# Kernel optimization log

Hardware: AMD Instinct MI355X
Metric: run time of the kernel (lower is better)

## Reference

```python
import jax, jax.numpy as jnp
import numpy as np

B, S, D, H = 2, 2048, 1024, 16
HD = D // H          # head dim = 64
BASE = 10000.0
SCALE = 1.0 / np.sqrt(HD)


def setup_inputs() -> dict:
    key = jax.random.key(0)
    ks = jax.random.split(key, 7)
    mk = lambda k, shp: (jax.random.normal(k, shp, dtype=jnp.float32) * 0.02)
    return {
        "hidden_states": jax.random.normal(ks[0], (B, S, D), dtype=jnp.float32),
        "Wq": mk(ks[1], (D, D)), "bq": jnp.zeros((D,), jnp.float32),
        "Wk": mk(ks[2], (D, D)), "bk": jnp.zeros((D,), jnp.float32),
        "Wv": mk(ks[3], (D, D)), "bv": jnp.zeros((D,), jnp.float32),
    }


def _rope_tables(seq_len, head_dim, dtype):
    # Intended RoPE: inv_freq over head_dim/2 frequencies.
    # (Original torch code has an off-by-2 indexing bug that makes it un-runnable
    #  for head_dim > 2; we implement the intended standard RoPE:
    #  inv_freq = base^{-arange(0, head_dim, 2)/head_dim}, length head_dim//2.)
    dim_half = head_dim // 2
    inv_freq = 1.0 / (BASE ** (jnp.arange(dim_half, dtype=dtype) / dim_half))
    ang = jnp.arange(seq_len, dtype=dtype)[:, None] * inv_freq[None, :]  # [S, dim_half]
    return jnp.sin(ang), jnp.cos(ang)


def _apply_rope(x, sin, cos):
    # x: [B, H, S, HD]; sin/cos: [S, HD//2]
    dim_half = x.shape[-1] // 2
    x1, x2 = x[..., :dim_half], x[..., dim_half:]
    sin = sin[None, None]  # [1,1,S,dim_half]
    cos = cos[None, None]
    return jnp.concatenate([x1 * cos - x2 * sin, x1 * sin + x2 * cos], axis=-1)


def reference(hidden_states, Wq, bq, Wk, bk, Wv, bv):
    b, s, d = hidden_states.shape
    # QKV projections (nn.Linear: x @ W.T + b), then split heads -> [B,H,S,HD]
    def proj(W, bias):
        y = jnp.einsum("bsd,ed->bse", hidden_states, W) + bias
        return y.reshape(b, s, H, HD).transpose(0, 2, 1, 3)

    q, k, v = proj(Wq, bq), proj(Wk, bk), proj(Wv, bv)

    sin, cos = _rope_tables(s, HD, hidden_states.dtype)
    q = _apply_rope(q, sin, cos)
    k = _apply_rope(k, sin, cos)

    # Non-causal SDPA, scale = 1/sqrt(head_dim), no mask, eval mode (no dropout)
    scores = jnp.einsum("bhqd,bhkd->bhqk", q, k) * SCALE
    probs = jax.nn.softmax(scores, axis=-1)
    ctx = jnp.einsum("bhqk,bhkd->bhqd", probs, v)

    # [B,H,S,HD] -> [B,S,D]
    return ctx.transpose(0, 2, 1, 3).reshape(b, s, d)
```

## Files before the change

kernel.cpp:

```cpp
#include <hip/hip_runtime.h>
#include <hip/hip_bf16.h>
#include <math.h>

#define B_  2
#define S_  2048
#define D_  1024
#define H_  16
#define HD_ 64
#define M_  (B_*S_)
#define N3  (3*D_)
#define K_  D_
#define LOG2E 1.44269504088896340736f

typedef unsigned short u16;
typedef __bf16 bf16x8 __attribute__((ext_vector_type(8)));
typedef float  f32x4  __attribute__((ext_vector_type(4)));
typedef float  f32x16 __attribute__((ext_vector_type(16)));
typedef unsigned short u16x4 __attribute__((ext_vector_type(4)));
typedef unsigned short u16x8 __attribute__((ext_vector_type(8)));
typedef unsigned int   u32x4v __attribute__((ext_vector_type(4)));

typedef const __attribute__((address_space(1))) unsigned int gu32;
typedef __attribute__((address_space(3)))       unsigned int lu32;

__device__ __forceinline__ void gload_lds16(const void* g, void* l) {
  __builtin_amdgcn_global_load_lds((gu32*)g, (lu32*)l, 16, 0, 0);
}

__device__ __forceinline__ u16 f2bf(float f) {
  unsigned u = __builtin_bit_cast(unsigned, f);
  u += 0x7fffu + ((u >> 16) & 1u);
  return (u16)(u >> 16);
}

__device__ __forceinline__ unsigned pk2(float lo, float hi) {
  unsigned d;
  asm("v_cvt_pk_bf16_f32 %0, %1, %2" : "=v"(d) : "v"(lo), "v"(hi));
  return d;
}

__global__ void k_prep(const float* __restrict__ hs, const float* __restrict__ Wq,
                       const float* __restrict__ Wk, const float* __restrict__ Wv,
                       u16* __restrict__ Xb, u16* __restrict__ Wb) {
  const int NX = M_*D_/4, NW = D_*D_/4;
  int i = blockIdx.x * blockDim.x + threadIdx.x;
  const float4* src; u16* dst; int off;
  if (i < NX)            { src = (const float4*)hs; dst = Xb;           off = i; }
  else if (i < NX+NW)    { src = (const float4*)Wq; dst = Wb;           off = i-NX; }
  else if (i < NX+2*NW)  { src = (const float4*)Wk; dst = Wb + D_*D_;   off = i-NX-NW; }
  else                   { src = (const float4*)Wv; dst = Wb + 2*D_*D_; off = i-NX-2*NW; }
  float4 v = src[off];
  ushort4 o; o.x = f2bf(v.x); o.y = f2bf(v.y); o.z = f2bf(v.z); o.w = f2bf(v.w);
  reinterpret_cast<ushort4*>(dst)[off] = o;
}

__global__ void k_tables(float* __restrict__ sinT, float* __restrict__ cosT) {
  int gid = blockIdx.x * blockDim.x + threadIdx.x;
  int s = gid >> 5, j = gid & 31;
  float invf = (float)exp(-(double)j * (log(10000.0) / 32.0));
  float angf = (float)s * invf;
  double ang = (double)angf;
  sinT[gid] = (float)sin(ang);
  cosT[gid] = (float)cos(ang);
}

#define BM 128
#define BN 128
#define BK 64

__global__ __launch_bounds__(256) void k_gemm(const u16* __restrict__ A,
                                              const u16* __restrict__ Bm,
                                              const float* __restrict__ bq,
                                              const float* __restrict__ bk,
                                              const float* __restrict__ bv,
                                              const float* __restrict__ sinT,
                                              const float* __restrict__ cosT,
                                              u16* __restrict__ Qo,
                                              u16* __restrict__ Ko,
                                              u16* __restrict__ Vo) {
  __shared__ alignas(16) u16 As[BM*BK];
  __shared__ alignas(16) u16 Bs[BN*BK];
  const int t = threadIdx.x;
  const int l = t & 63, w = t >> 6;
  const int wr = w >> 1, wc = w & 1;
  const int lr = l & 15, lg = l >> 4;
  const int m0 = blockIdx.y * BM, n0 = blockIdx.x * BN;

  f32x4 acc[4][4] = {};

  for (int k0 = 0; k0 < K_; k0 += BK) {
#pragma unroll
    for (int i = 0; i < 4; ++i) {
      int chunk = i*256 + t;
      int row = chunk >> 3, kc = chunk & 7;
      gload_lds16(A + (size_t)(m0+row)*K_ + k0 + kc*8, &As[chunk*8]);
    }
#pragma unroll
    for (int i = 0; i < 4; ++i) {
      int chunk = i*256 + t;
      int row = chunk >> 3, kc = chunk & 7;
      gload_lds16(Bm + (size_t)(n0+row)*K_ + k0 + kc*8, &Bs[chunk*8]);
    }
    __syncthreads();
#pragma unroll
    for (int ks = 0; ks < 2; ++ks) {
      bf16x8 a[4], b[4];
#pragma unroll
      for (int m = 0; m < 4; ++m)
        a[m] = *reinterpret_cast<const bf16x8*>(&As[(wr*64 + m*16 + lr)*BK + ks*32 + lg*8]);
#pragma unroll
      for (int n = 0; n < 4; ++n)
        b[n] = *reinterpret_cast<const bf16x8*>(&Bs[(wc*64 + n*16 + lr)*BK + ks*32 + lg*8]);
#pragma unroll
      for (int m = 0; m < 4; ++m)
#pragma unroll
        for (int n = 0; n < 4; ++n)
          acc[m][n] = __builtin_amdgcn_mfma_f32_16x16x32_bf16(a[m], b[n], acc[m][n], 0, 0, 0);
    }
    __syncthreads();
  }

  const int cw0  = n0 + wc*64;
  const int proj = cw0 >> 10;
  const int h    = (cw0 & (D_-1)) >> 6;
  const int b    = m0 >> 11;
  const int sb_  = (m0 & (S_-1)) + wr*64;

  if (proj < 2) {
    const float* bias = proj ? bk : bq;
    u16* dst = proj ? Ko : Qo;
    const float qs = proj ? 1.0f : 0.125f * LOG2E;
    float b1[2], b2[2];
#pragma unroll
    for (int n = 0; n < 2; ++n) {
      b1[n] = bias[h*HD_ + n*16 + lr];
      b2[n] = bias[h*HD_ + n*16 + lr + 32];
    }
#pragma unroll
    for (int m = 0; m < 4; ++m)
#pragma unroll
      for (int r = 0; r < 4; ++r) {
        int s = sb_ + m*16 + lg*4 + r;
        size_t orow = ((size_t)(b*H_ + h)*S_ + s)*HD_;
#pragma unroll
        for (int n = 0; n < 2; ++n) {
          int j = n*16 + lr;
          float x1 = acc[m][n][r]   + b1[n];
          float x2 = acc[m][n+2][r] + b2[n];
          float c  = cosT[(s<<5) + j], sn = sinT[(s<<5) + j];
          dst[orow + j]      = f2bf((x1*c - x2*sn) * qs);
          dst[orow + j + 32] = f2bf((x1*sn + x2*c) * qs);
        }
      }
  } else {
    float bb[4];
#pragma unroll
    for (int n = 0; n < 4; ++n) bb[n] = bv[h*HD_ + n*16 + lr];
#pragma unroll
    for (int m = 0; m < 4; ++m)
#pragma unroll
      for (int r = 0; r < 4; ++r) {
        int s = sb_ + m*16 + lg*4 + r;
        size_t orow = ((size_t)(b*H_ + h)*S_ + s)*HD_;
#pragma unroll
        for (int n = 0; n < 4; ++n)
          Vo[orow + n*16 + lr] = f2bf(acc[m][n][r] + bb[n]);
      }
  }
}

__global__ __launch_bounds__(256) void k_vt2(const u16* __restrict__ Vb,
                                             u16* __restrict__ Vt) {
  __shared__ u16 tile[64*68];
  const int bh = blockIdx.y, s0 = blockIdx.x * 64, t = threadIdx.x;
#pragma unroll
  for (int i = 0; i < 2; ++i) {
    int chunk = i*256 + t;
    int sl = chunk >> 3, c8 = chunk & 7;
    u16x8 v = *reinterpret_cast<const u16x8*>(Vb + ((size_t)bh*S_ + s0 + sl)*HD_ + c8*8);
    u16x4 lo = __builtin_shufflevector(v, v, 0, 1, 2, 3);
    u16x4 hi = __builtin_shufflevector(v, v, 4, 5, 6, 7);
    *reinterpret_cast<u16x4*>(&tile[sl*68 + c8*8])     = lo;
    *reinterpret_cast<u16x4*>(&tile[sl*68 + c8*8 + 4]) = hi;
  }
  __syncthreads();
#pragma unroll
  for (int i = 0; i < 2; ++i) {
    int chunk = i*256 + t;
    int hd = chunk >> 3, sb = chunk & 7;
    u16x8 o;
#pragma unroll
    for (int k = 0; k < 8; ++k) {
      int p   = sb*8 + k;
      int key = (p & ~15) | (p & 3) | ((p & 4) << 1) | ((p & 8) >> 1);
      o[k] = tile[key*68 + hd];
    }
    *reinterpret_cast<u16x8*>(Vt + ((size_t)bh*HD_ + hd)*S_ + s0 + sb*8) = o;
  }
}

#define QBW 32
#define NWV 4
#define QTT (QBW*NWV)
#define KTL 64
#define NTL (S_/KTL)

__global__ __launch_bounds__(256) void k_attn(const u16* __restrict__ Q,
                                              const u16* __restrict__ K,
                                              const u16* __restrict__ Vt,
                                              float* __restrict__ out) {
  __shared__ alignas(16) u16 Ks[2][KTL*HD_];
  __shared__ alignas(16) u16 Vs[2][HD_*KTL];
  __shared__ float lsums[NWV][QBW];
  const int t = threadIdx.x, l = t & 63, w = t >> 6;
  const int q32 = l & 31, hi = l >> 5;

  const int bid = blockIdx.x;
  const int work = (bid & 7) * 64 + (bid >> 3);
  const int bh = work >> 4;
  const int q0 = (work & 15) * QTT;

  const u16* Qg = Q  + ((size_t)bh*S_ + q0 + w*QBW)*HD_;
  const u16* Kg = K  + (size_t)bh*S_*HD_;
  const u16* Vg = Vt + (size_t)bh*HD_*S_;

  bf16x8 qf[4];
#pragma unroll
  for (int kt = 0; kt < 4; ++kt)
    qf[kt] = *reinterpret_cast<const bf16x8*>(Qg + (size_t)q32*HD_ + kt*16 + hi*8);

  f32x16 O0 = {}, O1 = {};
  float lsum = 0.f;

  const int srow = t >> 3, sg = t & 7;
  const int sg1 = sg ^ (srow & 7);
  const u16* kq = Kg + (size_t)srow*HD_ + sg1*8;
  const u16* vq = Vg + (size_t)srow*S_  + sg1*8;

  gload_lds16(kq,            &Ks[0][t*8]);
  gload_lds16(kq + 32*HD_,   &Ks[0][2048 + t*8]);
  gload_lds16(vq,            &Vs[0][t*8]);
  gload_lds16(vq + 32*S_,    &Vs[0][2048 + t*8]);
  __syncthreads();

  int cur = 0;
  for (int tile = 0; tile < NTL; ++tile) {
    if (tile + 1 < NTL) {
      const u16* kn = kq + (size_t)(tile+1)*KTL*HD_;
      const u16* vn = vq + (tile+1)*KTL;
      gload_lds16(kn,          &Ks[cur^1][t*8]);
      gload_lds16(kn + 32*HD_, &Ks[cur^1][2048 + t*8]);
      gload_lds16(vn,          &Vs[cur^1][t*8]);
      gload_lds16(vn + 32*S_,  &Vs[cur^1][2048 + t*8]);
    }

    f32x16 d0 = {}, d1 = {};
    __builtin_amdgcn_s_setprio(1);
#pragma unroll
    for (int kt = 0; kt < 4; ++kt) {
      const int gsw = ((kt*2 + hi) ^ (q32 & 7)) * 8;
      bf16x8 k0 = *reinterpret_cast<const bf16x8*>(&Ks[cur][q32*HD_ + gsw]);
      d0 = __builtin_amdgcn_mfma_f32_32x32x16_bf16(k0, qf[kt], d0, 0, 0, 0);
      bf16x8 k1 = *reinterpret_cast<const bf16x8*>(&Ks[cur][(32 + q32)*HD_ + gsw]);
      d1 = __builtin_amdgcn_mfma_f32_32x32x16_bf16(k1, qf[kt], d1, 0, 0, 0);
    }
    __builtin_amdgcn_s_setprio(0);

    unsigned pw[4][4];
#pragma unroll
    for (int c = 0; c < 4; ++c) {
      float e[8];
#pragma unroll
      for (int i = 0; i < 8; ++i) {
        float sv = (c < 2) ? d0[(c & 1)*8 + i] : d1[(c & 1)*8 + i];
        e[i] = exp2f(sv);
        lsum += e[i];
      }
#pragma unroll
      for (int j = 0; j < 4; ++j) pw[c][j] = pk2(e[2*j], e[2*j+1]);
    }

    __builtin_amdgcn_s_setprio(1);
#pragma unroll
    for (int c = 0; c < 4; ++c) {
      u32x4v pv_ = {pw[c][0], pw[c][1], pw[c][2], pw[c][3]};
      bf16x8 pa = __builtin_bit_cast(bf16x8, pv_);
      const int gv = ((c*2 + hi) ^ (q32 & 7)) * 8;
      bf16x8 v0 = *reinterpret_cast<const bf16x8*>(&Vs[cur][q32*KTL + gv]);
      O0 = __builtin_amdgcn_mfma_f32_32x32x16_bf16(pa, v0, O0, 0, 0, 0);
      bf16x8 v1 = *reinterpret_cast<const bf16x8*>(&Vs[cur][(32 + q32)*KTL + gv]);
      O1 = __builtin_amdgcn_mfma_f32_32x32x16_bf16(pa, v1, O1, 0, 0, 0);
    }
    __builtin_amdgcn_s_setprio(0);

    __syncthreads();
    cur ^= 1;
  }

  lsum += __shfl_xor(lsum, 32);
  if (l < 32) lsums[w][l] = lsum;

  const int b = bh >> 4, h = bh & 15;
#pragma unroll
  for (int r = 0; r < 16; ++r) {
    int qrow = (r & 3) + 8*(r >> 2) + 4*hi;
    float inv = 1.f / lsums[w][qrow];
    size_t o = (size_t)(b*S_ + q0 + w*QBW + qrow)*D_ + h*HD_;
    out[o + q32]      = O0[r] * inv;
    out[o + 32 + q32] = O1[r] * inv;
  }
}

extern "C" void kernel_launch(void* const* d_in, const int* in_sizes, int n_in,
                              void* d_out, int out_size, void* d_ws, size_t ws_size,
                              hipStream_t stream) {
  const float* hs = (const float*)d_in[0];
  const float* Wq = (const float*)d_in[1];
  const float* bq = (const float*)d_in[2];
  const float* Wk = (const float*)d_in[3];
  const float* bk = (const float*)d_in[4];
  const float* Wv = (const float*)d_in[5];
  const float* bv = (const float*)d_in[6];
  float* out = (float*)d_out;

  char* ws = (char*)d_ws;
  u16*   Xb   = (u16*)  (ws);
  u16*   Wb   = (u16*)  (ws + 8388608);
  u16*   Qb   = (u16*)  (ws + 14680064);
  u16*   Kb   = (u16*)  (ws + 23068672);
  u16*   Vb   = (u16*)  (ws + 31457280);
  u16*   Vtb  = (u16*)  (ws + 39845888);
  float* sinT = (float*)(ws + 48234496);
  float* cosT = (float*)(ws + 48496640);

  k_prep<<<(M_*D_/4 + 3*(D_*D_/4)) / 256, 256, 0, stream>>>(hs, Wq, Wk, Wv, Xb, Wb);
  k_tables<<<256, 256, 0, stream>>>(sinT, cosT);
  k_gemm<<<dim3(N3/BN, M_/BM), 256, 0, stream>>>(Xb, Wb, bq, bk, bv, sinT, cosT, Qb, Kb, Vb);
  k_vt2<<<dim3(S_/64, B_*H_), 256, 0, stream>>>(Vb, Vtb);
  k_attn<<<512, 256, 0, stream>>>(Qb, Kb, Vtb, out);
}
```

Before: 206.7 us.

## Double attention key tile to 128 and swizzle GEMM block order

```diff
diff --git a/kernel.cpp b/kernel.cpp
--- a/kernel.cpp
+++ b/kernel.cpp
@@ -84,7 +84,10 @@
   const int l = t & 63, w = t >> 6;
   const int wr = w >> 1, wc = w & 1;
   const int lr = l & 15, lg = l >> 4;
-  const int m0 = blockIdx.y * BM, n0 = blockIdx.x * BN;
+
+  const int lin = blockIdx.y * (N3/BN) + blockIdx.x;
+  const int wk  = (lin & 7) * 96 + (lin >> 3);
+  const int m0 = (wk / (N3/BN)) * BM, n0 = (wk % (N3/BN)) * BN;
 
   f32x4 acc[4][4] = {};
 
@@ -202,7 +205,7 @@
 #define QBW 32
 #define NWV 4
 #define QTT (QBW*NWV)
-#define KTL 64
+#define KTL 128
 #define NTL (S_/KTL)
 
 __global__ __launch_bounds__(256) void k_attn(const u16* __restrict__ Q,
@@ -232,66 +235,74 @@
   f32x16 O0 = {}, O1 = {};
   float lsum = 0.f;
 
-  const int srow = t >> 3, sg = t & 7;
-  const int sg1 = sg ^ (srow & 7);
-  const u16* kq = Kg + (size_t)srow*HD_ + sg1*8;
-  const u16* vq = Vg + (size_t)srow*S_  + sg1*8;
-
-  gload_lds16(kq,            &Ks[0][t*8]);
-  gload_lds16(kq + 32*HD_,   &Ks[0][2048 + t*8]);
-  gload_lds16(vq,            &Vs[0][t*8]);
-  gload_lds16(vq + 32*S_,    &Vs[0][2048 + t*8]);
+  const u16* ksrc[4]; const u16* vsrc[4];
+#pragma unroll
+  for (int i = 0; i < 4; ++i) {
+    int g  = t + 256*i;
+    int kr = g >> 3,  kc = (g & 7)  ^ (kr & 7);
+    ksrc[i] = Kg + (size_t)kr*HD_ + kc*8;
+    int vr = g >> 4,  vc = (g & 15) ^ (vr & 15);
+    vsrc[i] = Vg + (size_t)vr*S_ + vc*8;
+  }
+
+#pragma unroll
+  for (int i = 0; i < 4; ++i) {
+    gload_lds16(ksrc[i], &Ks[0][(t + 256*i)*8]);
+    gload_lds16(vsrc[i], &Vs[0][(t + 256*i)*8]);
+  }
   __syncthreads();
 
   int cur = 0;
   for (int tile = 0; tile < NTL; ++tile) {
     if (tile + 1 < NTL) {
-      const u16* kn = kq + (size_t)(tile+1)*KTL*HD_;
-      const u16* vn = vq + (tile+1)*KTL;
-      gload_lds16(kn,          &Ks[cur^1][t*8]);
-      gload_lds16(kn + 32*HD_, &Ks[cur^1][2048 + t*8]);
-      gload_lds16(vn,          &Vs[cur^1][t*8]);
-      gload_lds16(vn + 32*S_,  &Vs[cur^1][2048 + t*8]);
-    }
-
-    f32x16 d0 = {}, d1 = {};
-    __builtin_amdgcn_s_setprio(1);
-#pragma unroll
-    for (int kt = 0; kt < 4; ++kt) {
-      const int gsw = ((kt*2 + hi) ^ (q32 & 7)) * 8;
-      bf16x8 k0 = *reinterpret_cast<const bf16x8*>(&Ks[cur][q32*HD_ + gsw]);
-      d0 = __builtin_amdgcn_mfma_f32_32x32x16_bf16(k0, qf[kt], d0, 0, 0, 0);
-      bf16x8 k1 = *reinterpret_cast<const bf16x8*>(&Ks[cur][(32 + q32)*HD_ + gsw]);
-      d1 = __builtin_amdgcn_mfma_f32_32x32x16_bf16(k1, qf[kt], d1, 0, 0, 0);
-    }
-    __builtin_amdgcn_s_setprio(0);
-
-    unsigned pw[4][4];
-#pragma unroll
-    for (int c = 0; c < 4; ++c) {
-      float e[8];
-#pragma unroll
-      for (int i = 0; i < 8; ++i) {
-        float sv = (c < 2) ? d0[(c & 1)*8 + i] : d1[(c & 1)*8 + i];
-        e[i] = exp2f(sv);
-        lsum += e[i];
-      }
-#pragma unroll
-      for (int j = 0; j < 4; ++j) pw[c][j] = pk2(e[2*j], e[2*j+1]);
-    }
-
-    __builtin_amdgcn_s_setprio(1);
-#pragma unroll
-    for (int c = 0; c < 4; ++c) {
-      u32x4v pv_ = {pw[c][0], pw[c][1], pw[c][2], pw[c][3]};
-      bf16x8 pa = __builtin_bit_cast(bf16x8, pv_);
-      const int gv = ((c*2 + hi) ^ (q32 & 7)) * 8;
-      bf16x8 v0 = *reinterpret_cast<const bf16x8*>(&Vs[cur][q32*KTL + gv]);
-      O0 = __builtin_amdgcn_mfma_f32_32x32x16_bf16(pa, v0, O0, 0, 0, 0);
-      bf16x8 v1 = *reinterpret_cast<const bf16x8*>(&Vs[cur][(32 + q32)*KTL + gv]);
-      O1 = __builtin_amdgcn_mfma_f32_32x32x16_bf16(pa, v1, O1, 0, 0, 0);
-    }
-    __builtin_amdgcn_s_setprio(0);
+#pragma unroll
+      for (int i = 0; i < 4; ++i) {
+        gload_lds16(ksrc[i] + (size_t)(tile+1)*KTL*HD_, &Ks[cur^1][(t + 256*i)*8]);
+        gload_lds16(vsrc[i] + (tile+1)*KTL,             &Vs[cur^1][(t + 256*i)*8]);
+      }
+    }
+
+#pragma unroll
+    for (int half = 0; half < 2; ++half) {
+      f32x16 d0 = {}, d1 = {};
+      __builtin_amdgcn_s_setprio(1);
+#pragma unroll
+      for (int kt = 0; kt < 4; ++kt) {
+        const int gsw = ((kt*2 + hi) ^ (q32 & 7)) * 8;
+        bf16x8 k0 = *reinterpret_cast<const bf16x8*>(&Ks[cur][(half*64 + q32)*HD_ + gsw]);
+        d0 = __builtin_amdgcn_mfma_f32_32x32x16_bf16(k0, qf[kt], d0, 0, 0, 0);
+        bf16x8 k1 = *reinterpret_cast<const bf16x8*>(&Ks[cur][(half*64 + 32 + q32)*HD_ + gsw]);
+        d1 = __builtin_amdgcn_mfma_f32_32x32x16_bf16(k1, qf[kt], d1, 0, 0, 0);
+      }
+      __builtin_amdgcn_s_setprio(0);
+
+      unsigned pw[4][4];
+#pragma unroll
+      for (int c = 0; c < 4; ++c) {
+        float e[8];
+#pragma unroll
+        for (int i = 0; i < 8; ++i) {
+          float sv = (c < 2) ? d0[(c & 1)*8 + i] : d1[(c & 1)*8 + i];
+          e[i] = exp2f(sv);
+          lsum += e[i];
+        }
+#pragma unroll
+        for (int j = 0; j < 4; ++j) pw[c][j] = pk2(e[2*j], e[2*j+1]);
+      }
+
+      __builtin_amdgcn_s_setprio(1);
+#pragma unroll
+      for (int c = 0; c < 4; ++c) {
+        u32x4v pv_ = {pw[c][0], pw[c][1], pw[c][2], pw[c][3]};
+        bf16x8 pa = __builtin_bit_cast(bf16x8, pv_);
+        const int gv = ((half*8 + c*2 + hi) ^ (q32 & 15)) * 8;
+        bf16x8 v0 = *reinterpret_cast<const bf16x8*>(&Vs[cur][q32*KTL + gv]);
+        O0 = __builtin_amdgcn_mfma_f32_32x32x16_bf16(pa, v0, O0, 0, 0, 0);
+        bf16x8 v1 = *reinterpret_cast<const bf16x8*>(&Vs[cur][(32 + q32)*KTL + gv]);
+        O1 = __builtin_amdgcn_mfma_f32_32x32x16_bf16(pa, v1, O1, 0, 0, 0);
+      }
+      __builtin_amdgcn_s_setprio(0);
+    }
 
     __syncthreads();
     cur ^= 1;
```

Result: no change. 205.8 us (-0.4%).
